# Performance work log

Hardware: AMD Instinct MI355X
Metric: run time of the kernel (lower is better)

## Reference

```python
import jax, jax.numpy as jnp
import numpy as np

DIM = 3            # point feature dim (xyz)
POS_HID = 64       # pos_mlp hidden
ATTN_HID = DIM * 4 # attn_mlp hidden (mult=4)
N_NBR = 16         # points per group
GROUPS = 512       # groups per batch element
MLP_D = N_NBR * DIM  # 48


def setup_inputs() -> dict:
    key = jax.random.key(0)
    ks = jax.random.split(key, 20)
    B = 32
    s = lambda *sh: 1.0 / np.sqrt(sh[0])
    inp = {
        "original_points": jax.random.normal(ks[0], (B, GROUPS, DIM), jnp.float32),
        "data": jax.random.normal(ks[1], (B, GROUPS, N_NBR, DIM), jnp.float32),
        # PointTransformerLayer params
        "w_qkv": jax.random.normal(ks[2], (DIM, DIM * 3), jnp.float32) * s(DIM),
        "pos_w1": jax.random.normal(ks[3], (3, POS_HID), jnp.float32) * s(3),
        "pos_b1": jnp.zeros((POS_HID,), jnp.float32),
        "pos_w2": jax.random.normal(ks[4], (POS_HID, DIM), jnp.float32) * s(POS_HID),
        "pos_b2": jnp.zeros((DIM,), jnp.float32),
        "attn_w1": jax.random.normal(ks[5], (DIM, ATTN_HID), jnp.float32) * s(DIM),
        "attn_b1": jnp.zeros((ATTN_HID,), jnp.float32),
        "attn_w2": jax.random.normal(ks[6], (ATTN_HID, DIM), jnp.float32) * s(ATTN_HID),
        "attn_b2": jnp.zeros((DIM,), jnp.float32),
        # downstream MLP params
        "mlp_w1": jax.random.normal(ks[7], (MLP_D, MLP_D), jnp.float32) * s(MLP_D),
        "mlp_b1": jnp.zeros((MLP_D,), jnp.float32),
        "mlp_w2": jax.random.normal(ks[8], (MLP_D, MLP_D), jnp.float32) * s(MLP_D),
        "mlp_b2": jnp.zeros((MLP_D,), jnp.float32),
        "mlp_w3": jax.random.normal(ks[9], (MLP_D, 1), jnp.float32) * s(MLP_D),
        "mlp_b3": jnp.zeros((1,), jnp.float32),
    }
    return inp


def reference(original_points, data, w_qkv, pos_w1, pos_b1, pos_w2, pos_b2,
              attn_w1, attn_b1, attn_w2, attn_b2,
              mlp_w1, mlp_b1, mlp_w2, mlp_b2, mlp_w3, mlp_b3):
    B, G, n, d = data.shape
    x = data.reshape(B * G, n, d)          # (BG, n, 3)
    pos = x[:, :, :3]                       # pos == features here (f=3)

    # Point-transformer vector attention
    qkv = x @ w_qkv                          # (BG, n, 9)
    q, k, v = jnp.split(qkv, 3, axis=-1)
    rel_pos = pos[:, :, None, :] - pos[:, None, :, :]              # (BG, n, n, 3)
    rel_emb = jax.nn.relu(rel_pos @ pos_w1 + pos_b1) @ pos_w2 + pos_b2  # (BG, n, n, 3)
    qk_rel = q[:, :, None, :] - k[:, None, :, :]                   # (BG, n, n, 3)
    v_ij = v[:, None, :, :] + rel_emb                              # (BG, n, n, 3)
    sim = jax.nn.relu((qk_rel + rel_emb) @ attn_w1 + attn_b1) @ attn_w2 + attn_b2
    attn = jax.nn.softmax(sim, axis=-2)                            # softmax over j
    agg = jnp.einsum('bijd,bijd->bid', attn, v_ij)                 # (BG, n, 3)

    # regroup into (B, 512, 48) exactly as stack(split(512, dim=0))
    sa = agg.reshape(B, G, n * d)
    h = jax.nn.relu(sa @ mlp_w1 + mlp_b1)
    h = jax.nn.relu(h @ mlp_w2 + mlp_b2)
    return h @ mlp_w3 + mlp_b3              # (B, 512, 1)
```

## Files before the change

### kernel.cpp

```cpp
#include <hip/hip_runtime.h>


typedef _Float16 h2 __attribute__((ext_vector_type(2)));
typedef _Float16 h8 __attribute__((ext_vector_type(8)));

#define AH_STRIDE 36
#define MW1_OFF  256
#define MW2_OFF 1408

union H8U { h8 v; h2 p[4]; unsigned u[4]; };

__device__ __forceinline__ h2 pkrtz(float a, float b) {
    return __builtin_bit_cast(h2, __builtin_amdgcn_cvt_pkrtz(a, b));
}
__device__ __forceinline__ h2 uash2(unsigned u) {
    return __builtin_bit_cast(h2, u);
}
__device__ __forceinline__ h2 hmax2(h2 a, h2 b) {
    return __builtin_elementwise_max(a, b);
}

#if __has_builtin(__builtin_amdgcn_fdot2)
__device__ __forceinline__ float dot2acc(h2 a, h2 b, float c) {
    return __builtin_amdgcn_fdot2(a, b, c, false);
}
#else
__device__ __forceinline__ float dot2acc(h2 a, h2 b, float c) {
    float d;
    asm("v_dot2_f32_f16 %0, %1, %2, %3"
        : "=v"(d)
        : "v"(__builtin_bit_cast(int, a)), "v"(__builtin_bit_cast(int, b)), "v"(c));
    return d;
}
#endif

__device__ __forceinline__ float dpp_add16(float x) {
    float s = x;
    int t;
    t = __builtin_amdgcn_update_dpp(0, __builtin_bit_cast(int, s), 0x121, 0xf, 0xf, false);
    s += __builtin_bit_cast(float, t);
    t = __builtin_amdgcn_update_dpp(0, __builtin_bit_cast(int, s), 0x122, 0xf, 0xf, false);
    s += __builtin_bit_cast(float, t);
    t = __builtin_amdgcn_update_dpp(0, __builtin_bit_cast(int, s), 0x124, 0xf, 0xf, false);
    s += __builtin_bit_cast(float, t);
    t = __builtin_amdgcn_update_dpp(0, __builtin_bit_cast(int, s), 0x128, 0xf, 0xf, false);
    s += __builtin_bit_cast(float, t);
    return s;
}

__global__ void wpack(const float* __restrict__ pw2, const float* __restrict__ aw1,
                      const float* __restrict__ ab1, const float* __restrict__ aw2,
                      const float* __restrict__ mw1, const float* __restrict__ mw2,
                      unsigned* __restrict__ ws) {
    const int t = threadIdx.x;
    const float L2E = 1.44269504f;
    if (blockIdx.x == 0) {
        if (t < 96) {
            const int hp = t & 31, c = t >> 5;
            ws[c*32+hp] = __builtin_bit_cast(unsigned, pkrtz(pw2[(2*hp)*3+c], pw2[(2*hp+1)*3+c]));
        } else if (t < 114) {
            const int idx = t - 96, r = idx / 6, gp = idx % 6;
            ws[96+r*6+gp] = __builtin_bit_cast(unsigned, pkrtz(aw1[r*12+2*gp], aw1[r*12+2*gp+1]));
        } else if (t < 120) {
            const int gp = t - 114;
            ws[114+gp] = __builtin_bit_cast(unsigned, pkrtz(ab1[2*gp], ab1[2*gp+1]));
        } else if (t < 138) {
            const int idx = t - 120, gp = idx / 3, c = idx % 3;
            ws[120+gp*3+c] = __builtin_bit_cast(unsigned,
                pkrtz(aw2[(2*gp)*3+c] * L2E, aw2[(2*gp+1)*3+c] * L2E));
        }
    }
    const int idx = blockIdx.x * 256 + t;
    if (idx < 1152) {
        const int cp = idx / 48, o = idx % 48;
        ws[MW1_OFF + idx] = __builtin_bit_cast(unsigned,
            pkrtz(mw1[(2*cp)*48+o], mw1[(2*cp+1)*48+o]));
        ws[MW2_OFF + idx] = __builtin_bit_cast(unsigned,
            pkrtz(mw2[(2*cp)*48+o], mw2[(2*cp+1)*48+o]));
    }
}

struct SmWave {
    float q4[64], k4[64], v4[64];
    float sa[48], h1[48];
    unsigned a1h[16 * AH_STRIDE];
    unsigned a2h[16 * AH_STRIDE];
};

__global__ __launch_bounds__(256, 6) void pt_main(
    const float* __restrict__ data,
    const float* __restrict__ wqkv,
    const float* __restrict__ pw1,
    const float* __restrict__ pb1,
    const float* __restrict__ pb2,
    const float* __restrict__ ab2,
    const float* __restrict__ mb1,
    const float* __restrict__ mb2,
    const float* __restrict__ mw3,
    const float* __restrict__ mb3,
    const unsigned* __restrict__ wsp,
    float* __restrict__ out)
{
    __shared__ __attribute__((aligned(16))) SmWave sm[4];

    const int tid = threadIdx.x;
    const int w   = tid >> 6;
    const int ln  = tid & 63;
    const int g   = blockIdx.x * 4 + w;
    SmWave& S = sm[w];

    const int p  = ln & 15;
    const float x0 = data[g*48 + p*3 + 0];
    const float x1 = data[g*48 + p*3 + 1];
    const float x2 = data[g*48 + p*3 + 2];

    if (ln < 48) {
        const int sec = ln >> 4;
        float* dst = (sec == 0) ? S.q4 : (sec == 1) ? S.k4 : S.v4;
        #pragma unroll
        for (int c = 0; c < 3; ++c) {
            dst[p*4+c] = fmaf(x0, wqkv[0*9 + sec*3 + c],
                         fmaf(x1, wqkv[1*9 + sec*3 + c],
                         x2 * wqkv[2*9 + sec*3 + c]));
        }
        dst[p*4+3] = 0.0f;
    }

    {
        const int qd = ln >> 4;
        const int hc = qd << 4;
        float s[16];
        #pragma unroll
        for (int c = 0; c < 16; ++c) {
            const int h = hc + c;
            s[c] = fmaf(x0, pw1[h], fmaf(x1, pw1[64+h], x2 * pw1[128+h]));
        }
        uint4 a1u0, a1u1, a2u0, a2u1;
        #pragma unroll
        for (int d = 0; d < 4; ++d) {
            const int c = d * 2;
            (&a1u0.x)[d] = __builtin_bit_cast(unsigned, pkrtz(s[c]   + pb1[hc+c],   s[c+1] + pb1[hc+c+1]));
            (&a1u1.x)[d] = __builtin_bit_cast(unsigned, pkrtz(s[8+c] + pb1[hc+8+c], s[9+c] + pb1[hc+9+c]));
            (&a2u0.x)[d] = __builtin_bit_cast(unsigned, pkrtz(s[c],   s[c+1]));
            (&a2u1.x)[d] = __builtin_bit_cast(unsigned, pkrtz(s[8+c], s[9+c]));
        }
        const int base = p * AH_STRIDE + (qd << 3);
        *(uint4*)&S.a1h[base]     = a1u0;
        *(uint4*)&S.a1h[base + 4] = a1u1;
        *(uint4*)&S.a2h[base]     = a2u0;
        *(uint4*)&S.a2h[base + 4] = a2u1;
    }
    __builtin_amdgcn_wave_barrier();

    const int j = p, q = ln >> 4;
    const float4 kv = *(const float4*)&S.k4[j*4];
    const float4 vv = *(const float4*)&S.v4[j*4];
    const h2 z2 = {(_Float16)0, (_Float16)0};
    const float L2E = 1.44269504f;
    const float mb_0 = ab2[0] * L2E, mb_1 = ab2[1] * L2E, mb_2 = ab2[2] * L2E;

    H8U ajr[8];
    #pragma unroll
    for (int cc = 0; cc < 8; ++cc)
        ajr[cc].v = *(const h8*)&S.a2h[j * AH_STRIDE + cc*4];

    #pragma unroll
    for (int half = 0; half < 2; ++half) {
        const int iA = q + 8*half, iB = iA + 4;

        float eA0 = pb2[0], eA1 = pb2[1], eA2 = pb2[2];
        float eB0 = pb2[0], eB1 = pb2[1], eB2 = pb2[2];
        #pragma unroll
        for (int cc = 0; cc < 8; ++cc) {
            H8U aiA, aiB;
            aiA.v = *(const h8*)&S.a1h[iA * AH_STRIDE + cc*4];
            aiB.v = *(const h8*)&S.a1h[iB * AH_STRIDE + cc*4];
            #pragma unroll
            for (int m = 0; m < 4; ++m) {
                const int hp = cc*4 + m;
                const h2 w0 = uash2(wsp[0*32+hp]);
                const h2 w1 = uash2(wsp[1*32+hp]);
                const h2 w2 = uash2(wsp[2*32+hp]);
                h2 rA = hmax2(aiA.p[m] - ajr[cc].p[m], z2);
                h2 rB = hmax2(aiB.p[m] - ajr[cc].p[m], z2);
                eA0 = dot2acc(rA, w0, eA0);
                eA1 = dot2acc(rA, w1, eA1);
                eA2 = dot2acc(rA, w2, eA2);
                eB0 = dot2acc(rB, w0, eB0);
                eB1 = dot2acc(rB, w1, eB1);
                eB2 = dot2acc(rB, w2, eB2);
            }
        }

        const float4 qA = *(const float4*)&S.q4[iA*4];
        const float4 qB = *(const float4*)&S.q4[iB*4];

        const float viA0 = vv.x + eA0, viA1 = vv.y + eA1, viA2 = vv.z + eA2;
        const float viB0 = vv.x + eB0, viB1 = vv.y + eB1, viB2 = vv.z + eB2;
        const float siA0 = qA.x - kv.x + eA0, siA1 = qA.y - kv.y + eA1, siA2 = qA.z - kv.z + eA2;
        const float siB0 = qB.x - kv.x + eB0, siB1 = qB.y - kv.y + eB1, siB2 = qB.z - kv.z + eB2;

        const h2 sAx = pkrtz(siA0, siA0), sAy = pkrtz(siA1, siA1), sAz = pkrtz(siA2, siA2);
        const h2 sBx = pkrtz(siB0, siB0), sBy = pkrtz(siB1, siB1), sBz = pkrtz(siB2, siB2);
        float mA0 = mb_0, mA1 = mb_1, mA2 = mb_2;
        float mB0 = mb_0, mB1 = mb_1, mB2 = mb_2;
        #pragma unroll
        for (int gp = 0; gp < 6; ++gp) {
            const h2 b1p = uash2(wsp[114+gp]);
            const h2 u0 = uash2(wsp[96+0*6+gp]);
            const h2 u1 = uash2(wsp[96+1*6+gp]);
            const h2 u2 = uash2(wsp[96+2*6+gp]);
            const h2 v0 = uash2(wsp[120+gp*3+0]);
            const h2 v1 = uash2(wsp[120+gp*3+1]);
            const h2 v2 = uash2(wsp[120+gp*3+2]);
            h2 accA = b1p, accB = b1p;
            accA = __builtin_elementwise_fma(sAx, u0, accA);
            accA = __builtin_elementwise_fma(sAy, u1, accA);
            accA = __builtin_elementwise_fma(sAz, u2, accA);
            accB = __builtin_elementwise_fma(sBx, u0, accB);
            accB = __builtin_elementwise_fma(sBy, u1, accB);
            accB = __builtin_elementwise_fma(sBz, u2, accB);
            h2 hA = hmax2(accA, z2), hB = hmax2(accB, z2);
            mA0 = dot2acc(hA, v0, mA0);
            mA1 = dot2acc(hA, v1, mA1);
            mA2 = dot2acc(hA, v2, mA2);
            mB0 = dot2acc(hB, v0, mB0);
            mB1 = dot2acc(hB, v1, mB1);
            mB2 = dot2acc(hB, v2, mB2);
        }

        const float pA0 = __builtin_amdgcn_exp2f(mA0);
        const float pA1 = __builtin_amdgcn_exp2f(mA1);
        const float pA2 = __builtin_amdgcn_exp2f(mA2);
        const float pB0 = __builtin_amdgcn_exp2f(mB0);
        const float pB1 = __builtin_amdgcn_exp2f(mB1);
        const float pB2 = __builtin_amdgcn_exp2f(mB2);

        const float nA0 = dpp_add16(pA0 * viA0);
        const float nA1 = dpp_add16(pA1 * viA1);
        const float nA2 = dpp_add16(pA2 * viA2);
        const float dA0 = dpp_add16(pA0);
        const float dA1 = dpp_add16(pA1);
        const float dA2 = dpp_add16(pA2);
        const float nB0 = dpp_add16(pB0 * viB0);
        const float nB1 = dpp_add16(pB1 * viB1);
        const float nB2 = dpp_add16(pB2 * viB2);
        const float dB0 = dpp_add16(pB0);
        const float dB1 = dpp_add16(pB1);
        const float dB2 = dpp_add16(pB2);

        if (j == 0) {
            S.sa[iA*3+0] = nA0 * __builtin_amdgcn_rcpf(dA0);
            S.sa[iA*3+1] = nA1 * __builtin_amdgcn_rcpf(dA1);
            S.sa[iA*3+2] = nA2 * __builtin_amdgcn_rcpf(dA2);
            S.sa[iB*3+0] = nB0 * __builtin_amdgcn_rcpf(dB0);
            S.sa[iB*3+1] = nB1 * __builtin_amdgcn_rcpf(dB1);
            S.sa[iB*3+2] = nB2 * __builtin_amdgcn_rcpf(dB2);
        }
    }
    __builtin_amdgcn_wave_barrier();

    if (ln < 48) {
        const int o = ln;
        float a0 = 0.f, a1 = 0.f;
        #pragma unroll
        for (int c = 0; c < 48; c += 4) {
            const float4 sa = *(const float4*)&S.sa[c];
            const h2 pa = pkrtz(sa.x, sa.y);
            const h2 pb = pkrtz(sa.z, sa.w);
            a0 = dot2acc(pa, uash2(wsp[MW1_OFF + (c>>1)*48 + o]), a0);
            a1 = dot2acc(pb, uash2(wsp[MW1_OFF + ((c>>1)+1)*48 + o]), a1);
        }
        S.h1[o] = fmaxf(a0 + a1 + mb1[o], 0.0f);
        __builtin_amdgcn_wave_barrier();
        float b0 = 0.f, b1 = 0.f;
        #pragma unroll
        for (int c = 0; c < 48; c += 4) {
            const float4 hh = *(const float4*)&S.h1[c];
            const h2 pa = pkrtz(hh.x, hh.y);
            const h2 pb = pkrtz(hh.z, hh.w);
            b0 = dot2acc(pa, uash2(wsp[MW2_OFF + (c>>1)*48 + o]), b0);
            b1 = dot2acc(pb, uash2(wsp[MW2_OFF + ((c>>1)+1)*48 + o]), b1);
        }
        const float h2v = fmaxf(b0 + b1 + mb2[o], 0.0f);
        const float fv = h2v * mw3[o];
        const float r = dpp_add16(fv);
        const int ri = __builtin_bit_cast(int, r);
        const float tot =
            __builtin_bit_cast(float, __builtin_amdgcn_readlane(ri, 0)) +
            __builtin_bit_cast(float, __builtin_amdgcn_readlane(ri, 16)) +
            __builtin_bit_cast(float, __builtin_amdgcn_readlane(ri, 32));
        if (o == 0) out[g] = tot + mb3[0];
    }
}

extern "C" void kernel_launch(void* const* d_in, const int* in_sizes, int n_in,
                              void* d_out, int out_size, void* d_ws, size_t ws_size,
                              hipStream_t stream) {
    const float* data = (const float*)d_in[1];
    unsigned* ws = (unsigned*)d_ws;
    const int groups = out_size;

    wpack<<<5, 256, 0, stream>>>(
        (const float*)d_in[5],
        (const float*)d_in[7],
        (const float*)d_in[8],
        (const float*)d_in[9],
        (const float*)d_in[11],
        (const float*)d_in[13],
        ws);

    pt_main<<<groups / 4, 256, 0, stream>>>(
        data,
        (const float*)d_in[2],
        (const float*)d_in[3],
        (const float*)d_in[4],
        (const float*)d_in[6],
        (const float*)d_in[10],
        (const float*)d_in[12],
        (const float*)d_in[14],
        (const float*)d_in[15],
        (const float*)d_in[16],
        ws,
        (float*)d_out);
}
```

Baseline: 136.6 us.

## Compute pos-MLP second layer with MFMA 16x16x32 f16 instead of dot2

Replaces the per-lane fdot2 loop that evaluates the relative-position MLP output layer with MFMA f16 instructions, using a transposed, zero-padded copy of pos_w2 prepared in the weight-setup kernel. Each of 16 iterations computes ReLU differences for one row i and feeds them through two MFMAs, with lanes selecting their own result rows. The goal is to move the heaviest inner dot-product work onto matrix cores. In exchange it performs redundant MFMA work (only a quarter of the results are kept per iteration), adds extra LDS reads, and increases register pressure.

```diff
diff --git a/kernel.cpp b/kernel.cpp
--- a/kernel.cpp
+++ b/kernel.cpp
@@ -3,10 +3,12 @@
 
 typedef _Float16 h2 __attribute__((ext_vector_type(2)));
 typedef _Float16 h8 __attribute__((ext_vector_type(8)));
+typedef float f32x4 __attribute__((ext_vector_type(4)));
 
 #define AH_STRIDE 36
 #define MW1_OFF  256
 #define MW2_OFF 1408
+#define AW2T_OFF 2560
 
 union H8U { h8 v; h2 p[4]; unsigned u[4]; };
 
@@ -78,6 +80,16 @@
         ws[MW2_OFF + idx] = __builtin_bit_cast(unsigned,
             pkrtz(mw2[(2*cp)*48+o], mw2[(2*cp+1)*48+o]));
     }
+    if (idx < 512) {
+        const int ch = idx >> 8, rem = idx & 255;
+        const int l = rem >> 2, d = rem & 3;
+        const int c = (l & 15) & 3;
+        const bool valid = c < 3;
+        const int h0 = ((l >> 4) * 8) + 2*d + 32*ch;
+        const float v0 = valid ? pw2[h0*3 + c] : 0.0f;
+        const float v1 = valid ? pw2[(h0+1)*3 + c] : 0.0f;
+        ws[AW2T_OFF + idx] = __builtin_bit_cast(unsigned, pkrtz(v0, v1));
+    }
 }
 
 struct SmWave {
@@ -159,38 +171,44 @@
     const float L2E = 1.44269504f;
     const float mb_0 = ab2[0] * L2E, mb_1 = ab2[1] * L2E, mb_2 = ab2[2] * L2E;
 
-    H8U ajr[8];
+    H8U af0, af1;
+    *(uint4*)&af0 = *(const uint4*)&wsp[AW2T_OFF + ln*4];
+    *(uint4*)&af1 = *(const uint4*)&wsp[AW2T_OFF + 256 + ln*4];
+    H8U b2c0, b2c1;
+    b2c0.v = *(const h8*)&S.a2h[j * AH_STRIDE + q*4];
+    b2c1.v = *(const h8*)&S.a2h[j * AH_STRIDE + q*4 + 16];
+
+    const f32x4 pb2v = {pb2[0], pb2[1], pb2[2], 0.0f};
+    float e[4][3];
     #pragma unroll
-    for (int cc = 0; cc < 8; ++cc)
-        ajr[cc].v = *(const h8*)&S.a2h[j * AH_STRIDE + cc*4];
+    for (int s = 0; s < 4; ++s) { e[s][0] = 0.f; e[s][1] = 0.f; e[s][2] = 0.f; }
+
+    #pragma unroll
+    for (int t = 0; t < 16; ++t) {
+        H8U r0, r1, d0, d1;
+        r0.v = *(const h8*)&S.a1h[t * AH_STRIDE + q*4];
+        r1.v = *(const h8*)&S.a1h[t * AH_STRIDE + q*4 + 16];
+        #pragma unroll
+        for (int m = 0; m < 4; ++m) {
+            d0.p[m] = hmax2(r0.p[m] - b2c0.p[m], z2);
+            d1.p[m] = hmax2(r1.p[m] - b2c1.p[m], z2);
+        }
+        f32x4 acc = __builtin_amdgcn_mfma_f32_16x16x32_f16(af0.v, d0.v, pb2v, 0, 0, 0);
+        acc = __builtin_amdgcn_mfma_f32_16x16x32_f16(af1.v, d1.v, acc, 0, 0, 0);
+        const int s = t >> 2;
+        const bool keep = (q == (t & 3));
+        e[s][0] = keep ? acc[0] : e[s][0];
+        e[s][1] = keep ? acc[1] : e[s][1];
+        e[s][2] = keep ? acc[2] : e[s][2];
+    }
 
     #pragma unroll
     for (int half = 0; half < 2; ++half) {
         const int iA = q + 8*half, iB = iA + 4;
-
-        float eA0 = pb2[0], eA1 = pb2[1], eA2 = pb2[2];
-        float eB0 = pb2[0], eB1 = pb2[1], eB2 = pb2[2];
-        #pragma unroll
-        for (int cc = 0; cc < 8; ++cc) {
-            H8U aiA, aiB;
-            aiA.v = *(const h8*)&S.a1h[iA * AH_STRIDE + cc*4];
-            aiB.v = *(const h8*)&S.a1h[iB * AH_STRIDE + cc*4];
-            #pragma unroll
-            for (int m = 0; m < 4; ++m) {
-                const int hp = cc*4 + m;
-                const h2 w0 = uash2(wsp[0*32+hp]);
-                const h2 w1 = uash2(wsp[1*32+hp]);
-                const h2 w2 = uash2(wsp[2*32+hp]);
-                h2 rA = hmax2(aiA.p[m] - ajr[cc].p[m], z2);
-                h2 rB = hmax2(aiB.p[m] - ajr[cc].p[m], z2);
-                eA0 = dot2acc(rA, w0, eA0);
-                eA1 = dot2acc(rA, w1, eA1);
-                eA2 = dot2acc(rA, w2, eA2);
-                eB0 = dot2acc(rB, w0, eB0);
-                eB1 = dot2acc(rB, w1, eB1);
-                eB2 = dot2acc(rB, w2, eB2);
-            }
-        }
+        const int ha = 2*half, hb = 2*half + 1;
+
+        const float eA0 = e[ha][0], eA1 = e[ha][1], eA2 = e[ha][2];
+        const float eB0 = e[hb][0], eB1 = e[hb][1], eB2 = e[hb][2];
 
         const float4 qA = *(const float4*)&S.q4[iA*4];
         const float4 qB = *(const float4*)&S.q4[iB*4];
```

Result: faster. 127.3 us (-6.8%).
